# Kernel tuning notes

Hardware: AMD Instinct MI355X
Metric: run time of the kernel (lower is better)

## Reference

```python
import math
import jax, jax.numpy as jnp
from jax import lax
import numpy as np

B, T, DIM = 2, 1024, 512
EXPAND, D_STATE, CONV_K, NUM_SCALES = 2, 16, 4, 3
D_INNER = EXPAND * DIM
DT_RANK = D_INNER // 16


def parallel_scan_log(log_coeffs, log_values):
    # h_t = a_t*h_{t-1} + b_t via Heinsen log-space scan
    a_star = jnp.cumsum(log_coeffs, axis=1)
    return jnp.exp(a_star + lax.cumlogsumexp(log_values - a_star, axis=1))


def selective_scan(x, dt, A, B_ssm, C_ssm, D_p):
    Bb, Tt, di = x.shape
    ds = A.shape[1]
    dt = jax.nn.softplus(dt)
    dA = jnp.exp(dt[..., None] * A[None, None])                    # (B,T,di,ds)
    dBx = dt[..., None] * B_ssm[:, :, None, :] * x[..., None]      # (B,T,di,ds)
    log_dA = jnp.log(jnp.maximum(dA, 1e-38)).reshape(Bb, Tt, di * ds)
    log_dBx = jnp.log(jnp.maximum(dBx, 1e-38)).reshape(Bb, Tt, di * ds)
    h = parallel_scan_log(log_dA, log_dBx).reshape(Bb, Tt, di, ds)
    return jnp.einsum('bts,btds->btd', C_ssm, h) + D_p * x


def ssm_core(x, conv_w, conv_b, xproj_w, dtproj_w, dtproj_b, A_log, D_p):
    di = x.shape[-1]
    # depthwise causal conv1d: left-pad K-1 (== torch pad K-1 both sides + truncate to T)
    xc = lax.conv_general_dilated(x.transpose(0, 2, 1), conv_w, (1,), [(CONV_K - 1, 0)],
                                  dimension_numbers=('NCH', 'OIH', 'NCH'),
                                  feature_group_count=di)
    xc = jax.nn.silu((xc + conv_b[None, :, None]).transpose(0, 2, 1))
    proj = xc @ xproj_w.T
    dt_raw = proj[..., :DT_RANK]
    B_ssm = proj[..., DT_RANK:DT_RANK + D_STATE]
    C_ssm = proj[..., DT_RANK + D_STATE:]
    dt = dt_raw @ dtproj_w.T + dtproj_b
    A = -jnp.exp(A_log)
    return selective_scan(xc, dt, A, B_ssm, C_ssm, D_p)


def downsample(x, stride):
    if stride == 1:
        return x
    Bb, Tt, Dd = x.shape
    Tt2 = Tt // stride * stride
    return x[:, :Tt2].reshape(Bb, Tt2 // stride, stride, Dd).mean(axis=2)


def upsample(x, T_target):
    Bb, T_src, Dd = x.shape
    if T_src == T_target:
        return x
    factor = math.ceil(T_target / T_src)
    x_up = jnp.repeat(x, factor, axis=1)[:, :T_target]
    if x_up.shape[1] < T_target:
        pad = jnp.broadcast_to(x_up[:, -1:], (Bb, T_target - x_up.shape[1], Dd))
        x_up = jnp.concatenate([x_up, pad], axis=1)
    return x_up


def forward(x, in_proj_w, conv_w, conv_b, xproj_w, dtproj_w, dtproj_b, A_log, D_p,
            scale_weights, cg_w1, cg_w2, out_proj_w, ln_gamma, ln_beta):
    Tt = x.shape[1]
    residual = x
    xz = x @ in_proj_w.T
    x_in, gate = xz[..., :D_INNER], xz[..., D_INNER:]
    outs = []
    for s in range(NUM_SCALES):
        x_s = downsample(x_in, 2 ** s)
        y_s = ssm_core(x_s, conv_w[s], conv_b[s], xproj_w[s], dtproj_w[s],
                       dtproj_b[s], A_log[s], D_p[s])
        outs.append(upsample(y_s, Tt))
    w = jax.nn.softmax(scale_weights)
    fused = sum(w[s] * outs[s] for s in range(NUM_SCALES))
    ctx = jnp.mean(jnp.stack(outs, axis=0), axis=0)
    cg = jax.nn.sigmoid(jax.nn.silu(ctx @ cg_w1.T) @ cg_w2.T)
    fused = fused * cg
    out = (fused * jax.nn.silu(gate)) @ out_proj_w.T
    y = out + residual
    mu = jnp.mean(y, axis=-1, keepdims=True)
    var = jnp.var(y, axis=-1, keepdims=True)
    return (y - mu) / jnp.sqrt(var + 1e-5) * ln_gamma + ln_beta


def setup_inputs():
    key = jax.random.key(0)
    ks = jax.random.split(key, 12)
    x = jax.random.normal(ks[0], (B, T, DIM), jnp.float32)
    in_proj_w = jax.random.normal(ks[1], (2 * D_INNER, DIM), jnp.float32) * (1.0 / math.sqrt(DIM))
    conv_w = jax.random.normal(ks[2], (NUM_SCALES, D_INNER, 1, CONV_K), jnp.float32) * 0.3
    conv_b = jax.random.normal(ks[3], (NUM_SCALES, D_INNER), jnp.float32) * 0.05
    xproj_w = jax.random.normal(ks[4], (NUM_SCALES, DT_RANK + 2 * D_STATE, D_INNER), jnp.float32) * 0.02
    dtproj_w = jax.random.normal(ks[5], (NUM_SCALES, D_INNER, DT_RANK), jnp.float32) * 0.05
    dtproj_b = jax.random.uniform(ks[6], (NUM_SCALES, D_INNER), jnp.float32,
                                  math.log(0.001), math.log(0.1))
    A_log = jnp.broadcast_to(jnp.log(jnp.arange(1, D_STATE + 1, dtype=jnp.float32)),
                             (NUM_SCALES, D_INNER, D_STATE))
    D_p = jnp.ones((NUM_SCALES, D_INNER), jnp.float32)
    scale_weights = jnp.ones((NUM_SCALES,), jnp.float32)
    cg_w1 = jax.random.normal(ks[7], (D_INNER // 2, D_INNER), jnp.float32) * (1.0 / math.sqrt(D_INNER))
    cg_w2 = jax.random.normal(ks[8], (D_INNER, D_INNER // 2), jnp.float32) * (1.0 / math.sqrt(D_INNER // 2))
    out_proj_w = jax.random.normal(ks[9], (DIM, D_INNER), jnp.float32) * (1.0 / math.sqrt(D_INNER))
    ln_gamma = jnp.ones((DIM,), jnp.float32)
    ln_beta = jnp.zeros((DIM,), jnp.float32)
    return {"x": x, "in_proj_w": in_proj_w, "conv_w": conv_w, "conv_b": conv_b,
            "xproj_w": xproj_w, "dtproj_w": dtproj_w, "dtproj_b": dtproj_b,
            "A_log": A_log, "D_p": D_p, "scale_weights": scale_weights,
            "cg_w1": cg_w1, "cg_w2": cg_w2, "out_proj_w": out_proj_w,
            "ln_gamma": ln_gamma, "ln_beta": ln_beta}


def reference(x, in_proj_w, conv_w, conv_b, xproj_w, dtproj_w, dtproj_b, A_log, D_p,
              scale_weights, cg_w1, cg_w2, out_proj_w, ln_gamma, ln_beta):
    return forward(x, in_proj_w, conv_w, conv_b, xproj_w, dtproj_w, dtproj_b, A_log,
                   D_p, scale_weights, cg_w1, cg_w2, out_proj_w, ln_gamma, ln_beta)
```

## Files before the change

kernel.cpp:

```cpp
#include <hip/hip_runtime.h>
#include <hip/hip_bf16.h>

#define BATCH   2
#define SEQ     1024
#define DIMSZ   512
#define DINNER  1024
#define DTRANK  64
#define DSTATE  16
#define CHUNK   32

typedef __hip_bfloat16 bf16;
typedef __attribute__((ext_vector_type(8))) short s8v;
typedef __attribute__((ext_vector_type(4))) float f4v;

__device__ __forceinline__ float sigmoidf_(float x) { return 1.f / (1.f + __expf(-x)); }
__device__ __forceinline__ float siluf_(float x) { return x * sigmoidf_(x); }
__device__ __forceinline__ void split2(float v, bf16& hi, bf16& lo) {
    hi = __float2bfloat16(v);
    lo = __float2bfloat16(v - __bfloat162float(hi));
}
__device__ __forceinline__ void split_store4(const float4 v,
                                             bf16* __restrict__ ph,
                                             bf16* __restrict__ pl) {
    union { bf16 b[4]; uint2 u; } H, L;
    split2(v.x, H.b[0], L.b[0]); split2(v.y, H.b[1], L.b[1]);
    split2(v.z, H.b[2], L.b[2]); split2(v.w, H.b[3], L.b[3]);
    *reinterpret_cast<uint2*>(ph) = H.u;
    *reinterpret_cast<uint2*>(pl) = L.u;
}

template <int ACT, bool ADD_RES, bool DT_MODE, bool CTX_A, bool GATE3>
__global__ __launch_bounds__(256) void mgemm_kernel(
    const float* __restrict__ A, int lda, int K,
    const float* __restrict__ W,
    const float* __restrict__ bias,
    const float* __restrict__ res,
    const float* __restrict__ gxz,
    const float* __restrict__ yy0,
    const float* __restrict__ yy1,
    const float* __restrict__ yy2,
    const float* __restrict__ swp,
    float* __restrict__ C, int N)
{
    __shared__ bf16 Ah[64][72], Al[64][72], Bh[64][72], Bl[64][72];

    const int m0 = blockIdx.x * 64;
    const int n0 = blockIdx.y * 64;
    const int tid = threadIdx.x;
    const int wave = tid >> 6;
    const int lane = tid & 63;
    const int wm = (wave >> 1) * 32;
    const int wn = (wave & 1) * 32;
    const int m16 = lane & 15;
    const int q   = lane >> 4;

    int scale = 0;
    if (DT_MODE) scale = (m0 < 2048) ? 0 : ((m0 < 3072) ? 1 : 2);
    const float* Wp = DT_MODE ? (W + (size_t)scale * 1024 * K) : W;
    const float* bias_p = (ACT == 3) ? (DT_MODE ? bias + (size_t)scale * N : bias) : nullptr;

    f4v acc[2][2];
#pragma unroll
    for (int i = 0; i < 2; i++)
#pragma unroll
        for (int j = 0; j < 2; j++)
#pragma unroll
            for (int r = 0; r < 4; r++) acc[i][j][r] = 0.f;

    const int cch = tid & 15;
    const int c4  = cch * 4;
    const int r0  = tid >> 4;

    const float* a0p[4]; const float* a1p[4]; const float* a2p[4];
#pragma unroll
    for (int p = 0; p < 4; p++) {
        int m = m0 + r0 + p * 16;
        if (CTX_A) {
            int b = m >> 10, t = m & 1023;
            a0p[p] = yy0 + (size_t)m * 1024 + c4;
            a1p[p] = yy1 + (size_t)((b << 9) + (t >> 1)) * 1024 + c4;
            a2p[p] = yy2 + (size_t)((b << 8) + (t >> 2)) * 1024 + c4;
        } else {
            a0p[p] = A + (size_t)m * lda + c4;
        }
    }
    const float* Bbase = Wp + (size_t)(n0 + r0) * K + c4;

    const int nkt = K >> 6;
    float4 ra[4], rb[4];
#pragma unroll
    for (int p = 0; p < 4; p++) {
        if (CTX_A) {
            float4 u = *reinterpret_cast<const float4*>(a0p[p]);
            float4 v = *reinterpret_cast<const float4*>(a1p[p]);
            float4 w = *reinterpret_cast<const float4*>(a2p[p]);
            ra[p] = make_float4((u.x + v.x + w.x) * (1.f / 3.f), (u.y + v.y + w.y) * (1.f / 3.f),
                                (u.z + v.z + w.z) * (1.f / 3.f), (u.w + v.w + w.w) * (1.f / 3.f));
        } else {
            ra[p] = *reinterpret_cast<const float4*>(a0p[p]);
        }
        rb[p] = *reinterpret_cast<const float4*>(Bbase + (size_t)(p * 16) * K);
    }

    for (int kt = 0; kt < nkt; kt++) {
        if (kt) __syncthreads();
#pragma unroll
        for (int p = 0; p < 4; p++) {
            int r = r0 + p * 16;
            split_store4(ra[p], &Ah[r][c4], &Al[r][c4]);
            split_store4(rb[p], &Bh[r][c4], &Bl[r][c4]);
        }
        __syncthreads();
        if (kt + 1 < nkt) {
            int off = (kt + 1) * 64;
#pragma unroll
            for (int p = 0; p < 4; p++) {
                if (CTX_A) {
                    float4 u = *reinterpret_cast<const float4*>(a0p[p] + off);
                    float4 v = *reinterpret_cast<const float4*>(a1p[p] + off);
                    float4 w = *reinterpret_cast<const float4*>(a2p[p] + off);
                    ra[p] = make_float4((u.x + v.x + w.x) * (1.f / 3.f), (u.y + v.y + w.y) * (1.f / 3.f),
                                        (u.z + v.z + w.z) * (1.f / 3.f), (u.w + v.w + w.w) * (1.f / 3.f));
                } else {
                    ra[p] = *reinterpret_cast<const float4*>(a0p[p] + off);
                }
                rb[p] = *reinterpret_cast<const float4*>(Bbase + off + (size_t)(p * 16) * K);
            }
        }
#pragma unroll
        for (int kk = 0; kk < 2; kk++) {
            const int col = kk * 32 + q * 8;
            s8v ah[2], al[2], bh[2], bl[2];
#pragma unroll
            for (int i = 0; i < 2; i++) {
                int ar = wm + i * 16 + m16;
                ah[i] = *reinterpret_cast<const s8v*>(&Ah[ar][col]);
                al[i] = *reinterpret_cast<const s8v*>(&Al[ar][col]);
                int br = wn + i * 16 + m16;
                bh[i] = *reinterpret_cast<const s8v*>(&Bh[br][col]);
                bl[i] = *reinterpret_cast<const s8v*>(&Bl[br][col]);
            }
#pragma unroll
            for (int i = 0; i < 2; i++)
#pragma unroll
                for (int j = 0; j < 2; j++) {
                    acc[i][j] = __builtin_amdgcn_mfma_f32_16x16x32_bf16(ah[i], bh[j], acc[i][j], 0, 0, 0);
                    acc[i][j] = __builtin_amdgcn_mfma_f32_16x16x32_bf16(al[i], bh[j], acc[i][j], 0, 0, 0);
                    acc[i][j] = __builtin_amdgcn_mfma_f32_16x16x32_bf16(ah[i], bl[j], acc[i][j], 0, 0, 0);
                }
        }
    }

    float e0 = 0.f, e1 = 0.f, e2 = 0.f, inv = 0.f;
    if (GATE3) {
        float s0 = swp[0], s1 = swp[1], s2 = swp[2];
        float mx = fmaxf(s0, fmaxf(s1, s2));
        e0 = __expf(s0 - mx); e1 = __expf(s1 - mx); e2 = __expf(s2 - mx);
        inv = 1.f / (e0 + e1 + e2);
    }

#pragma unroll
    for (int i = 0; i < 2; i++) {
#pragma unroll
        for (int j = 0; j < 2; j++) {
#pragma unroll
            for (int r = 0; r < 4; r++) {
                int gm = m0 + wm + i * 16 + q * 4 + r;
                int gn = n0 + wn + j * 16 + m16;
                float v = acc[i][j][r];
                if (ACT == 3) { v += bias_p[gn]; v = (v > 20.f) ? v : __logf(1.f + __expf(v)); }
                else if (ACT == 1) v = siluf_(v);
                else if (ACT == 2) v = sigmoidf_(v);
                if (GATE3) {
                    int b = gm >> 10, t = gm & 1023;
                    float f = (e0 * yy0[(size_t)gm * 1024 + gn]
                             + e1 * yy1[(size_t)((b << 9) + (t >> 1)) * 1024 + gn]
                             + e2 * yy2[(size_t)((b << 8) + (t >> 2)) * 1024 + gn]) * inv;
                    v = f * v * siluf_(gxz[(size_t)gm * 2048 + 1024 + gn]);
                } else if (ADD_RES) {
                    v += res[(size_t)gm * N + gn];
                }
                C[(size_t)gm * N + gn] = v;
            }
        }
    }
}

__global__ __launch_bounds__(256) void xproj_mfma_kernel(
    const float* __restrict__ A, const float* __restrict__ xw,
    float* __restrict__ pj)
{
    const int K = 1024;
    __shared__ bf16 Ah[64][72], Al[64][72], Bh[64][72], Bl[64][72];

    const int m0 = blockIdx.x * 64;
    const int n0 = blockIdx.y * 64;
    const int tid = threadIdx.x;
    const int wave = tid >> 6;
    const int lane = tid & 63;
    const int wm = (wave >> 1) * 32;
    const int wn = (wave & 1) * 32;
    const int m16 = lane & 15;
    const int q   = lane >> 4;

    const int scale = (m0 < 2048) ? 0 : ((m0 < 3072) ? 1 : 2);
    const float* Wp = xw + (size_t)scale * 96 * K;

    f4v acc[2][2];
#pragma unroll
    for (int i = 0; i < 2; i++)
#pragma unroll
        for (int j = 0; j < 2; j++)
#pragma unroll
            for (int r = 0; r < 4; r++) acc[i][j][r] = 0.f;

    const int cch = tid & 15;
    const int c4  = cch * 4;
    const int r0  = tid >> 4;

    const float* Abase = A + (size_t)(m0 + r0) * K + c4;
    const float* Bbase = Wp + (size_t)(n0 + r0) * K + c4;
    bool bok[4];
#pragma unroll
    for (int p = 0; p < 4; p++) bok[p] = (n0 + r0 + p * 16) < 96;

    const int nkt = K >> 6;
    float4 ra[4], rb[4];
    const float4 zero4 = make_float4(0.f, 0.f, 0.f, 0.f);
#pragma unroll
    for (int p = 0; p < 4; p++) {
        ra[p] = *reinterpret_cast<const float4*>(Abase + (size_t)(p * 16) * K);
        rb[p] = bok[p] ? *reinterpret_cast<const float4*>(Bbase + (size_t)(p * 16) * K) : zero4;
    }

    for (int kt = 0; kt < nkt; kt++) {
        if (kt) __syncthreads();
#pragma unroll
        for (int p = 0; p < 4; p++) {
            int r = r0 + p * 16;
            split_store4(ra[p], &Ah[r][c4], &Al[r][c4]);
            split_store4(rb[p], &Bh[r][c4], &Bl[r][c4]);
        }
        __syncthreads();
        if (kt + 1 < nkt) {
            int off = (kt + 1) * 64;
#pragma unroll
            for (int p = 0; p < 4; p++) {
                ra[p] = *reinterpret_cast<const float4*>(Abase + off + (size_t)(p * 16) * K);
                rb[p] = bok[p] ? *reinterpret_cast<const float4*>(Bbase + off + (size_t)(p * 16) * K) : zero4;
            }
        }
#pragma unroll
        for (int kk = 0; kk < 2; kk++) {
            const int col = kk * 32 + q * 8;
            s8v ah[2], al[2], bh[2], bl[2];
#pragma unroll
            for (int i = 0; i < 2; i++) {
                int ar = wm + i * 16 + m16;
                ah[i] = *reinterpret_cast<const s8v*>(&Ah[ar][col]);
                al[i] = *reinterpret_cast<const s8v*>(&Al[ar][col]);
                int br = wn + i * 16 + m16;
                bh[i] = *reinterpret_cast<const s8v*>(&Bh[br][col]);
                bl[i] = *reinterpret_cast<const s8v*>(&Bl[br][col]);
            }
#pragma unroll
            for (int i = 0; i < 2; i++)
#pragma unroll
                for (int j = 0; j < 2; j++) {
                    acc[i][j] = __builtin_amdgcn_mfma_f32_16x16x32_bf16(ah[i], bh[j], acc[i][j], 0, 0, 0);
                    acc[i][j] = __builtin_amdgcn_mfma_f32_16x16x32_bf16(al[i], bh[j], acc[i][j], 0, 0, 0);
                    acc[i][j] = __builtin_amdgcn_mfma_f32_16x16x32_bf16(ah[i], bl[j], acc[i][j], 0, 0, 0);
                }
        }
    }

#pragma unroll
    for (int i = 0; i < 2; i++) {
#pragma unroll
        for (int j = 0; j < 2; j++) {
            int gn = n0 + wn + j * 16 + m16;
            if (gn >= 96) continue;
#pragma unroll
            for (int r = 0; r < 4; r++) {
                int gm = m0 + wm + i * 16 + q * 4 + r;
                pj[(size_t)gm * 96 + gn] = acc[i][j][r];
            }
        }
    }
}

__global__ void conv_fused_kernel(const float* __restrict__ xz,
                                  const float* __restrict__ cw,
                                  const float* __restrict__ cb,
                                  float* __restrict__ xc)
{
    int idx = blockIdx.x * blockDim.x + threadIdx.x;
    if (idx >= 3670016) return;
    int s, rel;
    if (idx < 2097152)      { s = 0; rel = idx; }
    else if (idx < 3145728) { s = 1; rel = idx - 2097152; }
    else                    { s = 2; rel = idx - 3145728; }
    int c = rel & 1023;
    int row = rel >> 10;
    int Ts = 1024 >> s;
    int b = row / Ts;
    int t = row - b * Ts;
    const float* base = xz + (size_t)(b * 1024) * 2048 + c;

    float acc = cb[s * 1024 + c];
#pragma unroll
    for (int k = 0; k < 4; k++) {
        int tau = t - 3 + k;
        if (tau < 0) continue;
        float xv;
        if (s == 0) {
            xv = base[(size_t)tau * 2048];
        } else if (s == 1) {
            xv = 0.5f * (base[(size_t)(2 * tau) * 2048] + base[(size_t)(2 * tau + 1) * 2048]);
        } else {
            xv = 0.25f * (base[(size_t)(4 * tau) * 2048] + base[(size_t)(4 * tau + 1) * 2048]
                        + base[(size_t)(4 * tau + 2) * 2048] + base[(size_t)(4 * tau + 3) * 2048]);
        }
        acc = fmaf(cw[(s * 1024 + c) * 4 + k], xv, acc);
    }
    xc[idx] = siluf_(acc);
}

__device__ __forceinline__ void scan_decode(int blk, int& s, int& nchunk, int& Ts,
                                            int& dquad, int& chunk, int& b, size_t& soff)
{
    int local;
    if (blk < 256)      { s = 0; local = blk;       soff = 0; }
    else if (blk < 384) { s = 1; local = blk - 256; soff = 1048576; }
    else                { s = 2; local = blk - 384; soff = 1572864; }
    nchunk = 32 >> s;
    Ts = 1024 >> s;
    dquad = local & 3;
    chunk = (local >> 2) & (nchunk - 1);
    b = local >> (7 - s);
}

__global__ __launch_bounds__(256) void scan_pass1(
    const float* __restrict__ dt0, const float* __restrict__ xc0, const float* __restrict__ pj0,
    const float* __restrict__ dt1, const float* __restrict__ xc1, const float* __restrict__ pj1,
    const float* __restrict__ dt2, const float* __restrict__ xc2, const float* __restrict__ pj2,
    const float* __restrict__ A_log,
    float* __restrict__ prodA_buf, float* __restrict__ h_buf)
{
    int s, nchunk, Ts, dquad, chunk, b; size_t soff;
    scan_decode(blockIdx.x, s, nchunk, Ts, dquad, chunk, b, soff);
    const float* dt = (s == 0) ? dt0 : (s == 1) ? dt1 : dt2;
    const float* xc = (s == 0) ? xc0 : (s == 1) ? xc1 : xc2;
    const float* pj = (s == 0) ? pj0 : (s == 1) ? pj1 : pj2;

    const int d = dquad * 256 + threadIdx.x;
    const size_t rowbase = (size_t)b * Ts;
    const int t0 = chunk * CHUNK;

    float Acoef[16], h[16], p[16];
#pragma unroll
    for (int j = 0; j < 16; j++) {
        Acoef[j] = -__expf(A_log[((size_t)(s * DINNER + d)) * 16 + j]);
        h[j] = 0.f; p[j] = 1.f;
    }

    __shared__ float bcB[CHUNK][16];
    for (int u = threadIdx.x; u < CHUNK * 16; u += 256) {
        int i = u >> 4, jj = u & 15;
        bcB[i][jj] = pj[(rowbase + t0 + i) * 96 + 64 + jj];
    }
    __syncthreads();

    for (int i = 0; i < CHUNK; i++) {
        size_t t = rowbase + t0 + i;
        float dtv = dt[t * DINNER + d];
        float xv  = xc[t * DINNER + d];
#pragma unroll
        for (int j = 0; j < 16; j++) {
            float dA  = fmaxf(__expf(dtv * Acoef[j]), 1e-38f);
            float dbx = fmaxf(dtv * bcB[i][j] * xv, 1e-38f);
            h[j] = fmaf(dA, h[j], dbx);
            p[j] *= dA;
        }
    }

    size_t base = soff + (size_t)((b * nchunk + chunk) * 16) * 1024 + d;
#pragma unroll
    for (int j = 0; j < 16; j++) {
        prodA_buf[base + (size_t)j * 1024] = p[j];
        h_buf[base + (size_t)j * 1024] = h[j];
    }
}

__global__ __launch_bounds__(256) void scan_pass2(
    const float* __restrict__ dt0, const float* __restrict__ xc0,
    const float* __restrict__ pj0, float* __restrict__ y0,
    const float* __restrict__ dt1, const float* __restrict__ xc1,
    const float* __restrict__ pj1, float* __restrict__ y1,
    const float* __restrict__ dt2, const float* __restrict__ xc2,
    const float* __restrict__ pj2, float* __restrict__ y2,
    const float* __restrict__ A_log, const float* __restrict__ D_p,
    const float* __restrict__ prodA_buf, const float* __restrict__ h_buf)
{
    int s, nchunk, Ts, dquad, chunk, b; size_t soff;
    scan_decode(blockIdx.x, s, nchunk, Ts, dquad, chunk, b, soff);
    const float* dt = (s == 0) ? dt0 : (s == 1) ? dt1 : dt2;
    const float* xc = (s == 0) ? xc0 : (s == 1) ? xc1 : xc2;
    const float* pj = (s == 0) ? pj0 : (s == 1) ? pj1 : pj2;
    float* y        = (s == 0) ? y0  : (s == 1) ? y1  : y2;

    const int d = dquad * 256 + threadIdx.x;
    const size_t rowbase = (size_t)b * Ts;
    const int t0 = chunk * CHUNK;

    float Acoef[16], h[16];
#pragma unroll
    for (int j = 0; j < 16; j++) {
        Acoef[j] = -__expf(A_log[((size_t)(s * DINNER + d)) * 16 + j]);
        h[j] = 0.f;
    }
    const float Dp = D_p[s * DINNER + d];

    for (int c = 0; c < chunk; c++) {
        size_t cb = soff + (size_t)((b * nchunk + c) * 16) * 1024 + d;
#pragma unroll
        for (int j = 0; j < 16; j++)
            h[j] = fmaf(prodA_buf[cb + (size_t)j * 1024], h[j], h_buf[cb + (size_t)j * 1024]);
    }

    __shared__ float bc[CHUNK][32];
    for (int u = threadIdx.x; u < CHUNK * 32; u += 256) {
        int i = u >> 5, jj = u & 31;
        bc[i][jj] = pj[(rowbase + t0 + i) * 96 + 64 + jj];
    }
    __syncthreads();

    for (int i = 0; i < CHUNK; i++) {
        size_t t = rowbase + t0 + i;
        float dtv = dt[t * DINNER + d];
        float xv  = xc[t * DINNER + d];
        float accy = 0.f;
#pragma unroll
        for (int j = 0; j < 16; j++) {
            float dA  = fmaxf(__expf(dtv * Acoef[j]), 1e-38f);
            float dbx = fmaxf(dtv * bc[i][j] * xv, 1e-38f);
            h[j] = fmaf(dA, h[j], dbx);
            accy = fmaf(bc[i][16 + j], h[j], accy);
        }
        y[t * DINNER + d] = accy + Dp * xv;
    }
}

__global__ __launch_bounds__(256) void ln_kernel(
    const float* __restrict__ yin, const float* __restrict__ gamma,
    const float* __restrict__ beta, float* __restrict__ out)
{
    int token = blockIdx.x;
    int tid = threadIdx.x;
    const float* row = yin + (size_t)token * DIMSZ;
    float v0 = row[tid], v1 = row[tid + 256];
    __shared__ float s1[256], s2[256];
    s1[tid] = v0 + v1;
    s2[tid] = v0 * v0 + v1 * v1;
    __syncthreads();
    for (int off = 128; off > 0; off >>= 1) {
        if (tid < off) { s1[tid] += s1[tid + off]; s2[tid] += s2[tid + off]; }
        __syncthreads();
    }
    float mu = s1[0] * (1.f / 512.f);
    float var = s2[0] * (1.f / 512.f) - mu * mu;
    float rstd = rsqrtf(var + 1e-5f);
    float* orow = out + (size_t)token * DIMSZ;
    orow[tid]       = (v0 - mu) * rstd * gamma[tid]       + beta[tid];
    orow[tid + 256] = (v1 - mu) * rstd * gamma[tid + 256] + beta[tid + 256];
}

extern "C" void kernel_launch(void* const* d_in, const int* in_sizes, int n_in,
                              void* d_out, int out_size, void* d_ws, size_t ws_size,
                              hipStream_t stream)
{
    const float* x         = (const float*)d_in[0];
    const float* in_proj_w = (const float*)d_in[1];
    const float* conv_w    = (const float*)d_in[2];
    const float* conv_b    = (const float*)d_in[3];
    const float* xproj_w   = (const float*)d_in[4];
    const float* dtproj_w  = (const float*)d_in[5];
    const float* dtproj_b  = (const float*)d_in[6];
    const float* A_log     = (const float*)d_in[7];
    const float* D_p       = (const float*)d_in[8];
    const float* scale_w   = (const float*)d_in[9];
    const float* cg_w1     = (const float*)d_in[10];
    const float* cg_w2     = (const float*)d_in[11];
    const float* out_pw    = (const float*)d_in[12];
    const float* ln_gamma  = (const float*)d_in[13];
    const float* ln_beta   = (const float*)d_in[14];
    float* out = (float*)d_out;

    float* ws = (float*)d_ws;
    float* xz    = ws;
    float* xc0   = xz    + 4194304;
    float* xc1   = xc0   + 2097152;
    float* xc2   = xc1   + 1048576;
    float* pj0   = xc2   + 524288;
    float* pj1   = pj0   + 196608;
    float* pj2   = pj1   + 98304;
    float* dt0   = pj2   + 49152;
    float* dt1   = dt0   + 2097152;
    float* dt2   = dt1   + 1048576;
    float* y0    = dt2   + 524288;
    float* y1    = y0    + 2097152;
    float* y2    = y1    + 1048576;
    float* prodA = y2    + 524288;
    float* hbuf  = prodA + 1835008;

    float* h1     = dt1;
    float* fusedg = dt0;
    float* outpre = xc1;

    mgemm_kernel<0, false, false, false, false><<<dim3(32, 32), 256, 0, stream>>>(
        x, DIMSZ, DIMSZ, in_proj_w, nullptr, nullptr, nullptr,
        nullptr, nullptr, nullptr, nullptr, xz, 2048);

    conv_fused_kernel<<<14336, 256, 0, stream>>>(xz, conv_w, conv_b, xc0);

    xproj_mfma_kernel<<<dim3(56, 2), 256, 0, stream>>>(xc0, xproj_w, pj0);

    mgemm_kernel<3, false, true, false, false><<<dim3(56, 16), 256, 0, stream>>>(
        pj0, 96, DTRANK, dtproj_w, dtproj_b, nullptr, nullptr,
        nullptr, nullptr, nullptr, nullptr, dt0, 1024);

    scan_pass1<<<448, 256, 0, stream>>>(dt0, xc0, pj0, dt1, xc1, pj1,
                                        dt2, xc2, pj2, A_log, prodA, hbuf);
    scan_pass2<<<448, 256, 0, stream>>>(dt0, xc0, pj0, y0, dt1, xc1, pj1, y1,
                                        dt2, xc2, pj2, y2, A_log, D_p, prodA, hbuf);

    mgemm_kernel<1, false, false, true, false><<<dim3(32, 8), 256, 0, stream>>>(
        nullptr, DINNER, DINNER, cg_w1, nullptr, nullptr, nullptr,
        y0, y1, y2, nullptr, h1, 512);

    mgemm_kernel<2, false, false, false, true><<<dim3(32, 16), 256, 0, stream>>>(
        h1, 512, 512, cg_w2, nullptr, nullptr, xz,
        y0, y1, y2, scale_w, fusedg, 1024);

    mgemm_kernel<0, true, false, false, false><<<dim3(32, 8), 256, 0, stream>>>(
        fusedg, DINNER, DINNER, out_pw, nullptr, x, nullptr,
        nullptr, nullptr, nullptr, nullptr, outpre, 512);

    ln_kernel<<<BATCH * SEQ, 256, 0, stream>>>(outpre, ln_gamma, ln_beta, out);
}
```

Before: 287.2 us.

## Halve scan chunk size and add separate carry-propagation kernel between scan passes

Scan chunks shrink from 32 to 16 timesteps, which doubles the block count of both scan passes. A new scan_carry kernel computes prefix carries across chunks once, so pass2 loads a single carry instead of walking all earlier chunks serially. The dt/xc loads are also software-prefetched one step ahead. This adds a kernel launch and more workspace traffic for the carry buffers, and the carry kernel itself runs a serial loop over 64 chunks with only 96 blocks.

```diff
diff --git a/kernel.cpp b/kernel.cpp
--- a/kernel.cpp
+++ b/kernel.cpp
@@ -7,7 +7,7 @@
 #define DINNER  1024
 #define DTRANK  64
 #define DSTATE  16
-#define CHUNK   32
+#define CHUNK   16
 
 typedef __hip_bfloat16 bf16;
 typedef __attribute__((ext_vector_type(8))) short s8v;
@@ -330,14 +330,14 @@
                                             int& dquad, int& chunk, int& b, size_t& soff)
 {
     int local;
-    if (blk < 256)      { s = 0; local = blk;       soff = 0; }
-    else if (blk < 384) { s = 1; local = blk - 256; soff = 1048576; }
-    else                { s = 2; local = blk - 384; soff = 1572864; }
-    nchunk = 32 >> s;
+    if (blk < 512)      { s = 0; local = blk;       soff = 0; }
+    else if (blk < 768) { s = 1; local = blk - 512; soff = 2097152; }
+    else                { s = 2; local = blk - 768; soff = 3145728; }
+    nchunk = 64 >> s;
     Ts = 1024 >> s;
     dquad = local & 3;
     chunk = (local >> 2) & (nchunk - 1);
-    b = local >> (7 - s);
+    b = local >> (8 - s);
 }
 
 __global__ __launch_bounds__(256) void scan_pass1(
@@ -365,16 +365,22 @@
     }
 
     __shared__ float bcB[CHUNK][16];
-    for (int u = threadIdx.x; u < CHUNK * 16; u += 256) {
-        int i = u >> 4, jj = u & 15;
+    if (threadIdx.x < CHUNK * 16) {
+        int i = threadIdx.x >> 4, jj = threadIdx.x & 15;
         bcB[i][jj] = pj[(rowbase + t0 + i) * 96 + 64 + jj];
     }
     __syncthreads();
 
+    size_t trow = (rowbase + t0) * DINNER + d;
+    float dtv = dt[trow];
+    float xv  = xc[trow];
     for (int i = 0; i < CHUNK; i++) {
-        size_t t = rowbase + t0 + i;
-        float dtv = dt[t * DINNER + d];
-        float xv  = xc[t * DINNER + d];
+        float dtn = 0.f, xvn = 0.f;
+        if (i + 1 < CHUNK) {
+            size_t tn = trow + (size_t)(i + 1) * DINNER;
+            dtn = dt[tn];
+            xvn = xc[tn];
+        }
 #pragma unroll
         for (int j = 0; j < 16; j++) {
             float dA  = fmaxf(__expf(dtv * Acoef[j]), 1e-38f);
@@ -382,6 +388,7 @@
             h[j] = fmaf(dA, h[j], dbx);
             p[j] *= dA;
         }
+        dtv = dtn; xv = xvn;
     }
 
     size_t base = soff + (size_t)((b * nchunk + chunk) * 16) * 1024 + d;
@@ -389,6 +396,32 @@
     for (int j = 0; j < 16; j++) {
         prodA_buf[base + (size_t)j * 1024] = p[j];
         h_buf[base + (size_t)j * 1024] = h[j];
+    }
+}
+
+__global__ __launch_bounds__(256) void scan_carry(
+    const float* __restrict__ prodA_buf, const float* __restrict__ h_buf,
+    float* __restrict__ c_buf)
+{
+    int s = blockIdx.x >> 5;
+    int local = blockIdx.x & 31;
+    int jq = local & 3;
+    int dquad = (local >> 2) & 3;
+    int b = local >> 4;
+    size_t soff = (s == 0) ? 0 : ((s == 1) ? 2097152 : 3145728);
+    int nchunk = 64 >> s;
+
+    const int d = dquad * 256 + threadIdx.x;
+    float H[4] = {0.f, 0.f, 0.f, 0.f};
+    for (int c = 0; c < nchunk; c++) {
+        size_t base = soff + (size_t)((b * nchunk + c) * 16 + jq * 4) * 1024 + d;
+#pragma unroll
+        for (int jj = 0; jj < 4; jj++) {
+            float p = prodA_buf[base + (size_t)jj * 1024];
+            float h = h_buf[base + (size_t)jj * 1024];
+            H[jj] = fmaf(p, H[jj], h);
+            c_buf[base + (size_t)jj * 1024] = H[jj];
+        }
     }
 }
 
@@ -400,7 +433,7 @@
     const float* __restrict__ dt2, const float* __restrict__ xc2,
     const float* __restrict__ pj2, float* __restrict__ y2,
     const float* __restrict__ A_log, const float* __restrict__ D_p,
-    const float* __restrict__ prodA_buf, const float* __restrict__ h_buf)
+    const float* __restrict__ c_buf)
 {
     int s, nchunk, Ts, dquad, chunk, b; size_t soff;
     scan_decode(blockIdx.x, s, nchunk, Ts, dquad, chunk, b, soff);
@@ -421,11 +454,11 @@
     }
     const float Dp = D_p[s * DINNER + d];
 
-    for (int c = 0; c < chunk; c++) {
-        size_t cb = soff + (size_t)((b * nchunk + c) * 16) * 1024 + d;
+    if (chunk > 0) {
+        size_t cb = soff + (size_t)((b * nchunk + chunk - 1) * 16) * 1024 + d;
 #pragma unroll
         for (int j = 0; j < 16; j++)
-            h[j] = fmaf(prodA_buf[cb + (size_t)j * 1024], h[j], h_buf[cb + (size_t)j * 1024]);
+            h[j] = c_buf[cb + (size_t)j * 1024];
     }
 
     __shared__ float bc[CHUNK][32];
@@ -435,10 +468,16 @@
     }
     __syncthreads();
 
+    size_t trow = (rowbase + t0) * DINNER + d;
+    float dtv = dt[trow];
+    float xv  = xc[trow];
     for (int i = 0; i < CHUNK; i++) {
-        size_t t = rowbase + t0 + i;
-        float dtv = dt[t * DINNER + d];
-        float xv  = xc[t * DINNER + d];
+        float dtn = 0.f, xvn = 0.f;
+        if (i + 1 < CHUNK) {
+            size_t tn = trow + (size_t)(i + 1) * DINNER;
+            dtn = dt[tn];
+            xvn = xc[tn];
+        }
         float accy = 0.f;
 #pragma unroll
         for (int j = 0; j < 16; j++) {
@@ -447,7 +486,8 @@
             h[j] = fmaf(dA, h[j], dbx);
             accy = fmaf(bc[i][16 + j], h[j], accy);
         }
-        y[t * DINNER + d] = accy + Dp * xv;
+        y[trow + (size_t)i * DINNER] = accy + Dp * xv;
+        dtv = dtn; xv = xvn;
     }
 }
 
@@ -511,7 +551,8 @@
     float* y1    = y0    + 2097152;
     float* y2    = y1    + 1048576;
     float* prodA = y2    + 524288;
-    float* hbuf  = prodA + 1835008;
+    float* hbuf  = prodA + 3670016;
+    float* cbuf  = hbuf  + 3670016;
 
     float* h1     = dt1;
     float* fusedg = dt0;
@@ -529,10 +570,11 @@
         pj0, 96, DTRANK, dtproj_w, dtproj_b, nullptr, nullptr,
         nullptr, nullptr, nullptr, nullptr, dt0, 1024);
 
-    scan_pass1<<<448, 256, 0, stream>>>(dt0, xc0, pj0, dt1, xc1, pj1,
+    scan_pass1<<<896, 256, 0, stream>>>(dt0, xc0, pj0, dt1, xc1, pj1,
                                         dt2, xc2, pj2, A_log, prodA, hbuf);
-    scan_pass2<<<448, 256, 0, stream>>>(dt0, xc0, pj0, y0, dt1, xc1, pj1, y1,
-                                        dt2, xc2, pj2, y2, A_log, D_p, prodA, hbuf);
+    scan_carry<<<96, 256, 0, stream>>>(prodA, hbuf, cbuf);
+    scan_pass2<<<896, 256, 0, stream>>>(dt0, xc0, pj0, y0, dt1, xc1, pj1, y1,
+                                        dt2, xc2, pj2, y2, A_log, D_p, cbuf);
 
     mgemm_kernel<1, false, false, true, false><<<dim3(32, 8), 256, 0, stream>>>(
         nullptr, DINNER, DINNER, cg_w1, nullptr, nullptr, nullptr,
```

Result: slower. 297.6 us (+3.6%).

## Split scan state dimension across two block halves and sum partial outputs

Applied to the files above, without the earlier changes.

Both scan passes now launch twice as many blocks, and each block handles 8 of the 16 SSM state channels. This halves the per-thread serial work and register state, and doubles the parallelism available to the latency-bound scan. Each half writes its own partial y buffer, so the downstream cross-gate GEMM and the gate epilogue now read and sum two buffers per scale. That doubles their y reads and adds workspace memory. The D skip term is added only by the first half.

```diff
diff --git a/kernel.cpp b/kernel.cpp
--- a/kernel.cpp
+++ b/kernel.cpp
@@ -36,9 +36,10 @@
     const float* __restrict__ bias,
     const float* __restrict__ res,
     const float* __restrict__ gxz,
-    const float* __restrict__ yy0,
-    const float* __restrict__ yy1,
-    const float* __restrict__ yy2,
+    const float* __restrict__ ya0, const float* __restrict__ ya1,
+    const float* __restrict__ ya2,
+    const float* __restrict__ yb0, const float* __restrict__ yb1,
+    const float* __restrict__ yb2,
     const float* __restrict__ swp,
     float* __restrict__ C, int N)
 {
@@ -71,15 +72,16 @@
     const int c4  = cch * 4;
     const int r0  = tid >> 4;
 
-    const float* a0p[4]; const float* a1p[4]; const float* a2p[4];
+    size_t off0[4], off1[4], off2[4];
+    const float* a0p[4];
 #pragma unroll
     for (int p = 0; p < 4; p++) {
         int m = m0 + r0 + p * 16;
         if (CTX_A) {
             int b = m >> 10, t = m & 1023;
-            a0p[p] = yy0 + (size_t)m * 1024 + c4;
-            a1p[p] = yy1 + (size_t)((b << 9) + (t >> 1)) * 1024 + c4;
-            a2p[p] = yy2 + (size_t)((b << 8) + (t >> 2)) * 1024 + c4;
+            off0[p] = (size_t)m * 1024 + c4;
+            off1[p] = (size_t)((b << 9) + (t >> 1)) * 1024 + c4;
+            off2[p] = (size_t)((b << 8) + (t >> 2)) * 1024 + c4;
         } else {
             a0p[p] = A + (size_t)m * lda + c4;
         }
@@ -91,11 +93,17 @@
 #pragma unroll
     for (int p = 0; p < 4; p++) {
         if (CTX_A) {
-            float4 u = *reinterpret_cast<const float4*>(a0p[p]);
-            float4 v = *reinterpret_cast<const float4*>(a1p[p]);
-            float4 w = *reinterpret_cast<const float4*>(a2p[p]);
-            ra[p] = make_float4((u.x + v.x + w.x) * (1.f / 3.f), (u.y + v.y + w.y) * (1.f / 3.f),
-                                (u.z + v.z + w.z) * (1.f / 3.f), (u.w + v.w + w.w) * (1.f / 3.f));
+            float4 u0 = *reinterpret_cast<const float4*>(ya0 + off0[p]);
+            float4 v0 = *reinterpret_cast<const float4*>(yb0 + off0[p]);
+            float4 u1 = *reinterpret_cast<const float4*>(ya1 + off1[p]);
+            float4 v1 = *reinterpret_cast<const float4*>(yb1 + off1[p]);
+            float4 u2 = *reinterpret_cast<const float4*>(ya2 + off2[p]);
+            float4 v2 = *reinterpret_cast<const float4*>(yb2 + off2[p]);
+            ra[p] = make_float4(
+                (u0.x + v0.x + u1.x + v1.x + u2.x + v2.x) * (1.f / 3.f),
+                (u0.y + v0.y + u1.y + v1.y + u2.y + v2.y) * (1.f / 3.f),
+                (u0.z + v0.z + u1.z + v1.z + u2.z + v2.z) * (1.f / 3.f),
+                (u0.w + v0.w + u1.w + v1.w + u2.w + v2.w) * (1.f / 3.f));
         } else {
             ra[p] = *reinterpret_cast<const float4*>(a0p[p]);
         }
@@ -116,11 +124,17 @@
 #pragma unroll
             for (int p = 0; p < 4; p++) {
                 if (CTX_A) {
-                    float4 u = *reinterpret_cast<const float4*>(a0p[p] + off);
-                    float4 v = *reinterpret_cast<const float4*>(a1p[p] + off);
-                    float4 w = *reinterpret_cast<const float4*>(a2p[p] + off);
-                    ra[p] = make_float4((u.x + v.x + w.x) * (1.f / 3.f), (u.y + v.y + w.y) * (1.f / 3.f),
-                                        (u.z + v.z + w.z) * (1.f / 3.f), (u.w + v.w + w.w) * (1.f / 3.f));
+                    float4 u0 = *reinterpret_cast<const float4*>(ya0 + off0[p] + off);
+                    float4 v0 = *reinterpret_cast<const float4*>(yb0 + off0[p] + off);
+                    float4 u1 = *reinterpret_cast<const float4*>(ya1 + off1[p] + off);
+                    float4 v1 = *reinterpret_cast<const float4*>(yb1 + off1[p] + off);
+                    float4 u2 = *reinterpret_cast<const float4*>(ya2 + off2[p] + off);
+                    float4 v2 = *reinterpret_cast<const float4*>(yb2 + off2[p] + off);
+                    ra[p] = make_float4(
+                        (u0.x + v0.x + u1.x + v1.x + u2.x + v2.x) * (1.f / 3.f),
+                        (u0.y + v0.y + u1.y + v1.y + u2.y + v2.y) * (1.f / 3.f),
+                        (u0.z + v0.z + u1.z + v1.z + u2.z + v2.z) * (1.f / 3.f),
+                        (u0.w + v0.w + u1.w + v1.w + u2.w + v2.w) * (1.f / 3.f));
                 } else {
                     ra[p] = *reinterpret_cast<const float4*>(a0p[p] + off);
                 }
@@ -173,9 +187,12 @@
                 else if (ACT == 2) v = sigmoidf_(v);
                 if (GATE3) {
                     int b = gm >> 10, t = gm & 1023;
-                    float f = (e0 * yy0[(size_t)gm * 1024 + gn]
-                             + e1 * yy1[(size_t)((b << 9) + (t >> 1)) * 1024 + gn]
-                             + e2 * yy2[(size_t)((b << 8) + (t >> 2)) * 1024 + gn]) * inv;
+                    size_t i0 = (size_t)gm * 1024 + gn;
+                    size_t i1 = (size_t)((b << 9) + (t >> 1)) * 1024 + gn;
+                    size_t i2 = (size_t)((b << 8) + (t >> 2)) * 1024 + gn;
+                    float f = (e0 * (ya0[i0] + yb0[i0])
+                             + e1 * (ya1[i1] + yb1[i1])
+                             + e2 * (ya2[i2] + yb2[i2])) * inv;
                     v = f * v * siluf_(gxz[(size_t)gm * 2048 + 1024 + gn]);
                 } else if (ADD_RES) {
                     v += res[(size_t)gm * N + gn];
@@ -347,8 +364,10 @@
     const float* __restrict__ A_log,
     float* __restrict__ prodA_buf, float* __restrict__ h_buf)
 {
+    const int jhalf = (blockIdx.x >= 448) ? 1 : 0;
+    const int jo = jhalf * 8;
     int s, nchunk, Ts, dquad, chunk, b; size_t soff;
-    scan_decode(blockIdx.x, s, nchunk, Ts, dquad, chunk, b, soff);
+    scan_decode(blockIdx.x - jhalf * 448, s, nchunk, Ts, dquad, chunk, b, soff);
     const float* dt = (s == 0) ? dt0 : (s == 1) ? dt1 : dt2;
     const float* xc = (s == 0) ? xc0 : (s == 1) ? xc1 : xc2;
     const float* pj = (s == 0) ? pj0 : (s == 1) ? pj1 : pj2;
@@ -357,17 +376,17 @@
     const size_t rowbase = (size_t)b * Ts;
     const int t0 = chunk * CHUNK;
 
-    float Acoef[16], h[16], p[16];
-#pragma unroll
-    for (int j = 0; j < 16; j++) {
-        Acoef[j] = -__expf(A_log[((size_t)(s * DINNER + d)) * 16 + j]);
+    float Acoef[8], h[8], p[8];
+#pragma unroll
+    for (int j = 0; j < 8; j++) {
+        Acoef[j] = -__expf(A_log[((size_t)(s * DINNER + d)) * 16 + jo + j]);
         h[j] = 0.f; p[j] = 1.f;
     }
 
-    __shared__ float bcB[CHUNK][16];
-    for (int u = threadIdx.x; u < CHUNK * 16; u += 256) {
-        int i = u >> 4, jj = u & 15;
-        bcB[i][jj] = pj[(rowbase + t0 + i) * 96 + 64 + jj];
+    __shared__ float bcB[CHUNK][8];
+    if (threadIdx.x < CHUNK * 8) {
+        int i = threadIdx.x >> 3, jj = threadIdx.x & 7;
+        bcB[i][jj] = pj[(rowbase + t0 + i) * 96 + 64 + jo + jj];
     }
     __syncthreads();
 
@@ -376,7 +395,7 @@
         float dtv = dt[t * DINNER + d];
         float xv  = xc[t * DINNER + d];
 #pragma unroll
-        for (int j = 0; j < 16; j++) {
+        for (int j = 0; j < 8; j++) {
             float dA  = fmaxf(__expf(dtv * Acoef[j]), 1e-38f);
             float dbx = fmaxf(dtv * bcB[i][j] * xv, 1e-38f);
             h[j] = fmaf(dA, h[j], dbx);
@@ -384,9 +403,9 @@
         }
     }
 
-    size_t base = soff + (size_t)((b * nchunk + chunk) * 16) * 1024 + d;
-#pragma unroll
-    for (int j = 0; j < 16; j++) {
+    size_t base = soff + (size_t)((b * nchunk + chunk) * 16 + jo) * 1024 + d;
+#pragma unroll
+    for (int j = 0; j < 8; j++) {
         prodA_buf[base + (size_t)j * 1024] = p[j];
         h_buf[base + (size_t)j * 1024] = h[j];
     }
@@ -394,44 +413,50 @@
 
 __global__ __launch_bounds__(256) void scan_pass2(
     const float* __restrict__ dt0, const float* __restrict__ xc0,
-    const float* __restrict__ pj0, float* __restrict__ y0,
+    const float* __restrict__ pj0,
     const float* __restrict__ dt1, const float* __restrict__ xc1,
-    const float* __restrict__ pj1, float* __restrict__ y1,
+    const float* __restrict__ pj1,
     const float* __restrict__ dt2, const float* __restrict__ xc2,
-    const float* __restrict__ pj2, float* __restrict__ y2,
+    const float* __restrict__ pj2,
+    float* __restrict__ ya0, float* __restrict__ ya1, float* __restrict__ ya2,
+    float* __restrict__ yb0, float* __restrict__ yb1, float* __restrict__ yb2,
     const float* __restrict__ A_log, const float* __restrict__ D_p,
     const float* __restrict__ prodA_buf, const float* __restrict__ h_buf)
 {
+    const int jhalf = (blockIdx.x >= 448) ? 1 : 0;
+    const int jo = jhalf * 8;
     int s, nchunk, Ts, dquad, chunk, b; size_t soff;
-    scan_decode(blockIdx.x, s, nchunk, Ts, dquad, chunk, b, soff);
+    scan_decode(blockIdx.x - jhalf * 448, s, nchunk, Ts, dquad, chunk, b, soff);
     const float* dt = (s == 0) ? dt0 : (s == 1) ? dt1 : dt2;
     const float* xc = (s == 0) ? xc0 : (s == 1) ? xc1 : xc2;
     const float* pj = (s == 0) ? pj0 : (s == 1) ? pj1 : pj2;
-    float* y        = (s == 0) ? y0  : (s == 1) ? y1  : y2;
+    float* y = jhalf ? ((s == 0) ? yb0 : (s == 1) ? yb1 : yb2)
+                     : ((s == 0) ? ya0 : (s == 1) ? ya1 : ya2);
 
     const int d = dquad * 256 + threadIdx.x;
     const size_t rowbase = (size_t)b * Ts;
     const int t0 = chunk * CHUNK;
 
-    float Acoef[16], h[16];
-#pragma unroll
-    for (int j = 0; j < 16; j++) {
-        Acoef[j] = -__expf(A_log[((size_t)(s * DINNER + d)) * 16 + j]);
+    float Acoef[8], h[8];
+#pragma unroll
+    for (int j = 0; j < 8; j++) {
+        Acoef[j] = -__expf(A_log[((size_t)(s * DINNER + d)) * 16 + jo + j]);
         h[j] = 0.f;
     }
-    const float Dp = D_p[s * DINNER + d];
+    const float Dp = (jhalf == 0) ? D_p[s * DINNER + d] : 0.f;
 
     for (int c = 0; c < chunk; c++) {
-        size_t cb = soff + (size_t)((b * nchunk + c) * 16) * 1024 + d;
-#pragma unroll
-        for (int j = 0; j < 16; j++)
+        size_t cb = soff + (size_t)((b * nchunk + c) * 16 + jo) * 1024 + d;
+#pragma unroll
+        for (int j = 0; j < 8; j++)
             h[j] = fmaf(prodA_buf[cb + (size_t)j * 1024], h[j], h_buf[cb + (size_t)j * 1024]);
     }
 
-    __shared__ float bc[CHUNK][32];
-    for (int u = threadIdx.x; u < CHUNK * 32; u += 256) {
-        int i = u >> 5, jj = u & 31;
-        bc[i][jj] = pj[(rowbase + t0 + i) * 96 + 64 + jj];
+    __shared__ float bc[CHUNK][16];
+    for (int u = threadIdx.x; u < CHUNK * 16; u += 256) {
+        int i = u >> 4, jj = u & 15;
+        int col = (jj < 8) ? (64 + jo + jj) : (80 + jo + (jj - 8));
+        bc[i][jj] = pj[(rowbase + t0 + i) * 96 + col];
     }
     __syncthreads();
 
@@ -441,11 +466,11 @@
         float xv  = xc[t * DINNER + d];
         float accy = 0.f;
 #pragma unroll
-        for (int j = 0; j < 16; j++) {
+        for (int j = 0; j < 8; j++) {
             float dA  = fmaxf(__expf(dtv * Acoef[j]), 1e-38f);
             float dbx = fmaxf(dtv * bc[i][j] * xv, 1e-38f);
             h[j] = fmaf(dA, h[j], dbx);
-            accy = fmaf(bc[i][16 + j], h[j], accy);
+            accy = fmaf(bc[i][8 + j], h[j], accy);
         }
         y[t * DINNER + d] = accy + Dp * xv;
     }
@@ -507,10 +532,13 @@
     float* dt0   = pj2   + 49152;
     float* dt1   = dt0   + 2097152;
     float* dt2   = dt1   + 1048576;
-    float* y0    = dt2   + 524288;
-    float* y1    = y0    + 2097152;
-    float* y2    = y1    + 1048576;
-    float* prodA = y2    + 524288;
+    float* ya0   = dt2   + 524288;
+    float* ya1   = ya0   + 2097152;
+    float* ya2   = ya1   + 1048576;
+    float* yb0   = ya2   + 524288;
+    float* yb1   = yb0   + 2097152;
+    float* yb2   = yb1   + 1048576;
+    float* prodA = yb2   + 524288;
     float* hbuf  = prodA + 1835008;
 
     float* h1     = dt1;
@@ -519,7 +547,7 @@
 
     mgemm_kernel<0, false, false, false, false><<<dim3(32, 32), 256, 0, stream>>>(
         x, DIMSZ, DIMSZ, in_proj_w, nullptr, nullptr, nullptr,
-        nullptr, nullptr, nullptr, nullptr, xz, 2048);
+        nullptr, nullptr, nullptr, nullptr, nullptr, nullptr, nullptr, xz, 2048);
 
     conv_fused_kernel<<<14336, 256, 0, stream>>>(xz, conv_w, conv_b, xc0);
 
@@ -527,24 +555,26 @@
 
     mgemm_kernel<3, false, true, false, false><<<dim3(56, 16), 256, 0, stream>>>(
         pj0, 96, DTRANK, dtproj_w, dtproj_b, nullptr, nullptr,
-        nullptr, nullptr, nullptr, nullptr, dt0, 1024);
-
-    scan_pass1<<<448, 256, 0, stream>>>(dt0, xc0, pj0, dt1, xc1, pj1,
+        nullptr, nullptr, nullptr, nullptr, nullptr, nullptr, nullptr, dt0, 1024);
+
+    scan_pass1<<<896, 256, 0, stream>>>(dt0, xc0, pj0, dt1, xc1, pj1,
                                         dt2, xc2, pj2, A_log, prodA, hbuf);
-    scan_pass2<<<448, 256, 0, stream>>>(dt0, xc0, pj0, y0, dt1, xc1, pj1, y1,
-                                        dt2, xc2, pj2, y2, A_log, D_p, prodA, hbuf);
+    scan_pass2<<<896, 256, 0, stream>>>(dt0, xc0, pj0, dt1, xc1, pj1,
+                                        dt2, xc2, pj2,
+                                        ya0, ya1, ya2, yb0, yb1, yb2,
+                                        A_log, D_p, prodA, hbuf);
 
     mgemm_kernel<1, false, false, true, false><<<dim3(32, 8), 256, 0, stream>>>(
         nullptr, DINNER, DINNER, cg_w1, nullptr, nullptr, nullptr,
-        y0, y1, y2, nullptr, h1, 512);
+        ya0, ya1, ya2, yb0, yb1, yb2, nullptr, h1, 512);
 
     mgemm_kernel<2, false, false, false, true><<<dim3(32, 16), 256, 0, stream>>>(
         h1, 512, 512, cg_w2, nullptr, nullptr, xz,
-        y0, y1, y2, scale_w, fusedg, 1024);
+        ya0, ya1, ya2, yb0, yb1, yb2, scale_w, fusedg, 1024);
 
     mgemm_kernel<0, true, false, false, false><<<dim3(32, 8), 256, 0, stream>>>(
         fusedg, DINNER, DINNER, out_pw, nullptr, x, nullptr,
-        nullptr, nullptr, nullptr, nullptr, outpre, 512);
+        nullptr, nullptr, nullptr, nullptr, nullptr, nullptr, nullptr, outpre, 512);
 
     ln_kernel<<<BATCH * SEQ, 256, 0, stream>>>(outpre, ln_gamma, ln_beta, out);
 }
```

New measurement: 296.3 us. 3.2% more time.
